# Optimization experiments

Hardware: AMD Instinct MI355X
Metric: run time of the kernel (lower is better)

## Reference

```python
import jax, jax.numpy as jnp
import numpy as np

INPUT_DIM, HIDDEN, EVENT_DIM = 64, 256, 32
B, T = 128, 1024


def setup_inputs() -> dict:
    key = jax.random.key(0)
    ks = jax.random.split(key, 20)
    s = 0.02
    return {
        "x": jax.random.normal(ks[0], (B, T, INPUT_DIM), jnp.float32),
        "events": jax.random.normal(ks[1], (B, T, EVENT_DIM), jnp.float32),
        "time_distances": jax.random.uniform(ks[2], (B, T), jnp.float32),
        # input projection
        "W_proj": s * jax.random.normal(ks[3], (INPUT_DIM, HIDDEN), jnp.float32),
        "b_proj": jnp.zeros((HIDDEN,), jnp.float32),
        # custom LSTM cell (input = projected_x of size HIDDEN)
        "W_ih": s * jax.random.normal(ks[4], (HIDDEN, 4 * HIDDEN), jnp.float32),
        "W_hh": s * jax.random.normal(ks[5], (HIDDEN, 4 * HIDDEN), jnp.float32),
        "b_lstm": jnp.zeros((4 * HIDDEN,), jnp.float32),
        # market-state gate from raw x
        "W_mk": s * jax.random.normal(ks[6], (INPUT_DIM, HIDDEN), jnp.float32),
        "b_mk": jnp.zeros((HIDDEN,), jnp.float32),
        # event processor
        "W_e": s * jax.random.normal(ks[7], (EVENT_DIM, HIDDEN), jnp.float32),
        "b_e": jnp.zeros((HIDDEN,), jnp.float32),
        "W_hg": s * jax.random.normal(ks[8], (HIDDEN, HIDDEN), jnp.float32),
        "b_hg": jnp.zeros((HIDDEN,), jnp.float32),
        "decay": jnp.asarray(0.5, jnp.float32),
        # predictor MLP (dropout is eval-mode identity)
        "W_p1": s * jax.random.normal(ks[9], (HIDDEN, HIDDEN // 2), jnp.float32),
        "b_p1": jnp.zeros((HIDDEN // 2,), jnp.float32),
        "W_p2": s * jax.random.normal(ks[10], (HIDDEN // 2, 1), jnp.float32),
        "b_p2": jnp.zeros((1,), jnp.float32),
    }


def _tmdo(x):
    # temporal first difference and Laplacian (second difference), zero-padded to [B,T,D]
    d1 = jnp.concatenate([jnp.zeros_like(x[:, :1]), x[:, 1:] - x[:, :-1]], axis=1)
    lap = jnp.concatenate(
        [jnp.zeros_like(x[:, :1]),
         x[:, 2:] - 2.0 * x[:, 1:-1] + x[:, :-2],
         jnp.zeros_like(x[:, :1])], axis=1)
    return d1, lap


def reference(x, events, time_distances, W_proj, b_proj, W_ih, W_hh, b_lstm,
              W_mk, b_mk, W_e, b_e, W_hg, b_hg, decay, W_p1, b_p1, W_p2, b_p2):
    bsz, seq_len, _ = x.shape
    H = W_proj.shape[1]
    tmdo_features, lap_features = _tmdo(x)

    h0 = jnp.zeros((bsz, H), x.dtype)
    c0 = jnp.zeros((bsz, H), x.dtype)

    def step(carry, inp):
        h, c = carry
        xt, et, dt = inp  # [B,D_in], [B,E], [B]
        px = xt @ W_proj + b_proj                                  # input_proj
        # event processor: embedded event * hidden gate * time decay
        e = jnp.tanh(et @ W_e + b_e)
        gate = jax.nn.sigmoid(h @ W_hg + b_hg)
        impact = e * gate * jnp.exp(-jax.nn.softplus(decay) * dt[:, None])
        # custom LSTM cell with market gate from raw x and event injection
        gates = px @ W_ih + h @ W_hh + b_lstm
        i_g, f_g, g_g, o_g = jnp.split(gates, 4, axis=-1)
        mk = jax.nn.sigmoid(xt @ W_mk + b_mk)
        c_new = jax.nn.sigmoid(f_g) * c + jax.nn.sigmoid(i_g) * jnp.tanh(g_g) \
                + mk * jnp.tanh(impact)
        h_new = jax.nn.sigmoid(o_g) * jnp.tanh(c_new)
        # predictor (exact GELU like torch nn.GELU; dropout = identity in eval)
        pred = jax.nn.gelu(h_new @ W_p1 + b_p1, approximate=False) @ W_p2 + b_p2
        return (h_new, c_new), (pred, h_new)

    xs = (jnp.swapaxes(x, 0, 1), jnp.swapaxes(events, 0, 1),
          jnp.swapaxes(time_distances, 0, 1))
    _, (preds, feats) = jax.lax.scan(step, (h0, c0), xs)
    predictions = jnp.swapaxes(preds, 0, 1)  # [B,T,1]
    features = jnp.swapaxes(feats, 0, 1)     # [B,T,H]
    return predictions, features, tmdo_features
```

## Files before the change

kernel.cpp:

```cpp
#include <hip/hip_runtime.h>
#include <hip/hip_bf16.h>
#include <hip/hip_fp16.h>
#include <math.h>

#define BB 128
#define TT 1024
#define DIN 64
#define HH 256
#define EE 32
#define BT (BB * TT)

typedef unsigned int uint;
typedef unsigned char uchar;
typedef _Float16 half2v __attribute__((ext_vector_type(2)));

__device__ __forceinline__ int dot4(uint a, uint b, int c) {
  return __builtin_amdgcn_sdot4((int)a, (int)b, c, false);
}
__device__ __forceinline__ uint pkh(float a, float b) {
  return __builtin_bit_cast(uint, __builtin_amdgcn_cvt_pkrtz(a, b));
}
__device__ __forceinline__ half2v uph(uint u) { return __builtin_bit_cast(half2v, u); }
__device__ __forceinline__ float fdot2u(uint a, uint b, float c) {
  return __builtin_amdgcn_fdot2(uph(a), uph(b), c, false);
}
#define IDPP(v, c) __builtin_amdgcn_mov_dpp((v), (c), 0xF, 0xF, true)
#define FDPP(v, c) __int_as_float(__builtin_amdgcn_mov_dpp(__float_as_int(v), (c), 0xF, 0xF, true))
__device__ __forceinline__ int qsum(int v) {
  v += IDPP(v, 0xB1);
  v += IDPP(v, 0x4E);
  return v;
}
__device__ __forceinline__ float rcp_f(float x) { return __builtin_amdgcn_rcpf(x); }
__device__ __forceinline__ float sigm(float x) { return rcp_f(1.0f + __expf(-x)); }
__device__ __forceinline__ float tanh_f(float x) {
  return 1.0f - 2.0f * rcp_f(__expf(2.0f * x) + 1.0f);
}

__global__ void fold_f32(const float* __restrict__ Wproj, const float* __restrict__ Wih,
                         float* __restrict__ Wfold) {
  int idx = blockIdx.x * blockDim.x + threadIdx.x;
  if (idx >= 64 * 1024) return;
  int d = idx >> 10, n = idx & 1023;
  float a = 0.f;
  for (int k = 0; k < 256; ++k) a += Wproj[d * 256 + k] * Wih[k * 1024 + n];
  Wfold[d * 1024 + n] = a;
}

__global__ void bfold_kernel(const float* __restrict__ bproj, const float* __restrict__ Wih,
                             const float* __restrict__ blstm, float* __restrict__ bfold) {
  int n = blockIdx.x * blockDim.x + threadIdx.x;
  if (n >= 1024) return;
  float a = blstm[n];
  for (int k = 0; k < 256; ++k) a += bproj[k] * Wih[k * 1024 + n];
  bfold[n] = a;
}

__global__ __launch_bounds__(1024) void quant_all(
    const float* __restrict__ Whh, const float* __restrict__ Whg,
    const float* __restrict__ Wfold, const float* __restrict__ Wmk,
    const float* __restrict__ We,
    uint* __restrict__ WhV, uint* __restrict__ WhL,
    uint* __restrict__ XQ, uint* __restrict__ EQ,
    float* __restrict__ scales) {
  const int bid = blockIdx.x, tid = threadIdx.x;
  const float* src;
  int nelem;
  switch (bid) {
    case 0: src = Whh;   nelem = 262144; break;
    case 1: src = Whg;   nelem = 65536;  break;
    case 2: src = Wfold; nelem = 65536;  break;
    case 3: src = Wmk;   nelem = 16384;  break;
    default: src = We;   nelem = 8192;   break;
  }
  float m = 0.f;
  for (int i = tid; i < nelem; i += 1024) m = fmaxf(m, fabsf(src[i]));
#pragma unroll
  for (int d = 1; d < 64; d <<= 1) m = fmaxf(m, __shfl_xor(m, d));
  __shared__ float wm[16];
  if ((tid & 63) == 0) wm[tid >> 6] = m;
  __syncthreads();
  float mg = wm[0];
#pragma unroll
  for (int i = 1; i < 16; ++i) mg = fmaxf(mg, wm[i]);
  mg = fmaxf(mg, 1e-8f);
  if (tid == 0) scales[bid] = mg * (1.0f / 127.0f);
  const float inv = 127.0f / mg;

  if (bid == 0) {
    for (int i = tid; i < 65536; i += 1024) {
      int C = i >> 4, r = i & 15;
      int c = C >> 2, q = C & 3, mI = r >> 2, mm = r & 3;
      int k4 = q * 16 + mI * 4 + mm;
      uint d = 0;
#pragma unroll
      for (int bb = 0; bb < 4; ++bb) {
        int qv = __float2int_rn(Whh[(4 * k4 + bb) * 1024 + c] * inv);
        qv = max(-127, min(127, qv));
        d |= ((uint)(qv & 0xff)) << (8 * bb);
      }
      WhV[i] = d;
    }
  } else if (bid == 1) {
    for (int i = tid; i < 16384; i += 1024) {
      int mm = i & 3, rest = i >> 2;
      int mI = rest >> 10, jq = rest & 1023;
      int j = jq >> 2, qq = jq & 3;
      int k4 = qq * 16 + mI * 4 + mm;
      uint d = 0;
#pragma unroll
      for (int bb = 0; bb < 4; ++bb) {
        int qv = __float2int_rn(Whg[(4 * k4 + bb) * 256 + j] * inv);
        qv = max(-127, min(127, qv));
        d |= ((uint)(qv & 0xff)) << (8 * bb);
      }
      WhL[i] = d;
    }
  } else if (bid == 2) {
    for (int i = tid; i < 16384; i += 1024) {
      int c = i >> 4, k4 = i & 15;
      uint d = 0;
#pragma unroll
      for (int bb = 0; bb < 4; ++bb) {
        int qv = __float2int_rn(Wfold[(4 * k4 + bb) * 1024 + c] * inv);
        qv = max(-127, min(127, qv));
        d |= ((uint)(qv & 0xff)) << (8 * bb);
      }
      XQ[i] = d;
    }
  } else if (bid == 3) {
    for (int i = tid; i < 4096; i += 1024) {
      int j = i >> 4, k4 = i & 15;
      uint d = 0;
#pragma unroll
      for (int bb = 0; bb < 4; ++bb) {
        int qv = __float2int_rn(Wmk[(4 * k4 + bb) * 256 + j] * inv);
        qv = max(-127, min(127, qv));
        d |= ((uint)(qv & 0xff)) << (8 * bb);
      }
      XQ[16384 + i] = d;
    }
  } else {
    for (int i = tid; i < 2048; i += 1024) {
      int c = i >> 3, k4 = i & 7;
      uint d = 0;
#pragma unroll
      for (int bb = 0; bb < 4; ++bb) {
        int qv = __float2int_rn(We[(4 * k4 + bb) * 256 + c] * inv);
        qv = max(-127, min(127, qv));
        d |= ((uint)(qv & 0xff)) << (8 * bb);
      }
      EQ[i] = d;
    }
  }
}

__global__ void pack_wp1h(const float* __restrict__ Wp1, uint* __restrict__ WQ) {
  int idx = blockIdx.x * blockDim.x + threadIdx.x;
  if (idx >= 16384) return;
  int j = idx >> 7, kp = idx & 127;
  WQ[idx] = pkh(Wp1[(2 * kp) * 128 + j], Wp1[(2 * kp + 1) * 128 + j]);
}

__global__ __launch_bounds__(256) void prep_inputs(
    const float* __restrict__ x, const float* __restrict__ ev, const float* __restrict__ td,
    const float* __restrict__ decay, uint* __restrict__ xq, uint* __restrict__ eq,
    float4* __restrict__ scl) {
  int wid = threadIdx.x >> 6, lane = threadIdx.x & 63;
  int bt = blockIdx.x * 4 + wid;
  if (bt >= BT) return;
  float xv = x[(size_t)bt * DIN + lane];
  float evv = (lane < EE) ? ev[(size_t)bt * EE + lane] : 0.0f;
  float ax = fabsf(xv), ae = fabsf(evv);
#pragma unroll
  for (int m = 1; m < 64; m <<= 1) {
    ax = fmaxf(ax, __shfl_xor(ax, m));
    ae = fmaxf(ae, __shfl_xor(ae, m));
  }
  float mgx = fmaxf(ax, 1e-8f), mge = fmaxf(ae, 1e-8f);
  int qx = __float2int_rn(xv * (127.0f / mgx));
  qx = max(-127, min(127, qx));
  int qe = __float2int_rn(evv * (127.0f / mge));
  qe = max(-127, min(127, qe));
  uint dx = 0, de = 0;
#pragma unroll
  for (int b = 0; b < 4; ++b) dx |= ((uint)(__shfl(qx, lane * 4 + b) & 0xff)) << (8 * b);
#pragma unroll
  for (int b = 0; b < 4; ++b) de |= ((uint)(__shfl(qe, lane * 4 + b) & 0xff)) << (8 * b);
  if (lane < 16) xq[(size_t)bt * 16 + lane] = dx;
  if (lane < 8) eq[(size_t)bt * 8 + lane] = de;
  if (lane == 0) {
    float sp = log1pf(__expf(decay[0]));
    scl[bt] = make_float4(mgx * (1.0f / 127.0f), mge * (1.0f / 127.0f),
                          __expf(-sp * td[bt]), 0.0f);
  }
}

__global__ void d1_kernel(const float* __restrict__ x, float* __restrict__ out2) {
  int idx = blockIdx.x * blockDim.x + threadIdx.x;
  const int per_t = DIN / 4;
  if (idx >= BB * TT * per_t) return;
  int t = (idx / per_t) % TT;
  float4 cur = reinterpret_cast<const float4*>(x)[idx];
  float4 res;
  if (t == 0) {
    res = make_float4(0.f, 0.f, 0.f, 0.f);
  } else {
    float4 prv = reinterpret_cast<const float4*>(x)[idx - per_t];
    res = make_float4(cur.x - prv.x, cur.y - prv.y, cur.z - prv.z, cur.w - prv.w);
  }
  reinterpret_cast<float4*>(out2)[idx] = res;
}

__global__ __launch_bounds__(1024) void pre_kernel(
    int t0, int lsteps,
    const uint* __restrict__ XQ, const uint* __restrict__ EQ,
    const float* __restrict__ scales, const float* __restrict__ bfold,
    const float* __restrict__ bmk, const float* __restrict__ be,
    const uint* __restrict__ xq, const uint* __restrict__ eqp,
    const float4* __restrict__ scl, uint4* __restrict__ pre) {
  const int tid = threadIdx.x;
  const int jj = tid >> 2, g = tid & 3;
  uint wx[16];
#pragma unroll
  for (int k = 0; k < 16; ++k) wx[k] = XQ[(g * 256 + jj) * 16 + k];
  uint wm[4];
#pragma unroll
  for (int k = 0; k < 4; ++k) wm[k] = XQ[16384 + jj * 16 + g * 4 + k];
  const uint we0 = EQ[jj * 8 + g * 2], we1 = EQ[jj * 8 + g * 2 + 1];
  const float sXF = scales[2], sMK = scales[3], sE = scales[4];
  const float bf = bfold[g * 256 + jj];
  const float bmkv = bmk[jj], bev = be[jj];
  const int steps = 1 << lsteps;

  for (int it = 0; it < 64; ++it) {
    const int idx = blockIdx.x * 64 + it;
    const int b = idx >> lsteps, tl = idx & (steps - 1);
    const int bt = b * TT + t0 + tl;
    const uint4* x4 = (const uint4*)(xq + (size_t)bt * 16);
    const uint4 X0 = x4[0], X1 = x4[1], X2 = x4[2], X3 = x4[3];
    const uint4 Xg = x4[g];
    const uint2 E0 = ((const uint2*)(eqp + (size_t)bt * 8))[g];
    const float4 sv = scl[bt];

    int ag = 0;
    ag = dot4(wx[0], X0.x, ag);  ag = dot4(wx[1], X0.y, ag);
    ag = dot4(wx[2], X0.z, ag);  ag = dot4(wx[3], X0.w, ag);
    ag = dot4(wx[4], X1.x, ag);  ag = dot4(wx[5], X1.y, ag);
    ag = dot4(wx[6], X1.z, ag);  ag = dot4(wx[7], X1.w, ag);
    ag = dot4(wx[8], X2.x, ag);  ag = dot4(wx[9], X2.y, ag);
    ag = dot4(wx[10], X2.z, ag); ag = dot4(wx[11], X2.w, ag);
    ag = dot4(wx[12], X3.x, ag); ag = dot4(wx[13], X3.y, ag);
    ag = dot4(wx[14], X3.z, ag); ag = dot4(wx[15], X3.w, ag);

    int am = 0;
    am = dot4(wm[0], Xg.x, am); am = dot4(wm[1], Xg.y, am);
    am = dot4(wm[2], Xg.z, am); am = dot4(wm[3], Xg.w, am);
    int ae = dot4(we0, E0.x, 0);
    ae = dot4(we1, E0.y, ae);
    am = qsum(am);
    ae = qsum(ae);

    const float p = (float)ag * (sXF * sv.x) + bf;
    const float p1 = FDPP(p, 0x55);
    const float p2 = FDPP(p, 0xAA);
    const float p3 = FDPP(p, 0xFF);
    if (g == 0) {
      const float mkS = sigm((float)am * (sMK * sv.x) + bmkv);
      const float ge = (float)ae * (sE * sv.y) + bev;
      const float EF = tanh_f(ge) * sv.z;
      uint4 o;
      o.x = pkh(p, p1);
      o.y = pkh(p2, p3);
      o.z = __float_as_uint(mkS);
      o.w = __float_as_uint(EF);
      pre[(size_t)idx * 256 + jj] = o;
    }
  }
}

__attribute__((amdgpu_waves_per_eu(4, 4)))
__global__ __launch_bounds__(1024) void scan3(
    int t0, int steps,
    const uint* __restrict__ WhV, const uint* __restrict__ WhLg,
    const float* __restrict__ scales, const float* __restrict__ bhg,
    const uint4* __restrict__ pre, uchar* __restrict__ hB, float* __restrict__ cB,
    float* __restrict__ feat) {
  __shared__ __align__(16) uint WL[16384];
  __shared__ __align__(16) uint hqW[128];
  const int tid = threadIdx.x, b = blockIdx.x;
  const int j = tid >> 2, q = tid & 3;

  for (int i = tid; i < 4096; i += 1024) ((uint4*)WL)[i] = ((const uint4*)WhLg)[i];

  uint4 wh[4][4];
  const uint4* wv = (const uint4*)WhV;
#pragma unroll
  for (int g = 0; g < 4; ++g)
#pragma unroll
    for (int m = 0; m < 4; ++m) wh[g][m] = wv[(g * 1024 + tid) * 4 + m];

  float c;
  if (t0 == 0) {
    c = 0.0f;
    if (tid < 64) hqW[tid] = 0u;
  } else {
    c = cB[b * 256 + j];
    if (tid < 64) hqW[tid] = ((const uint*)hB)[b * 64 + tid];
  }
  const float kHH = scales[0] * (1.0f / 127.0f);
  const float kHG = scales[1] * (1.0f / 127.0f);
  const float bhgv = bhg[j];
  const uint4* prep = pre + (size_t)b * steps * 256;
  float* fout = feat + ((size_t)b * TT + t0) * HH;
  const uint4* WL4 = (const uint4*)WL;
  int buf = 0;
  __syncthreads();

  uint4 P = prep[j];
  for (int t = 0; t < steps; ++t) {
    uint4 Pn = P;
    if (t + 1 < steps) Pn = prep[(size_t)(t + 1) * 256 + j];

    int a0 = 0, a1 = 0, a2 = 0, a3 = 0, a4 = 0;
    const uint4* hp = (const uint4*)((const uchar*)hqW + buf * 256 + q * 64);
#pragma unroll
    for (int m = 0; m < 4; ++m) {
      const uint4 hv = hp[m];
      const uint4 wg = WL4[m * 1024 + tid];
      a0 = dot4(wh[0][m].x, hv.x, a0); a0 = dot4(wh[0][m].y, hv.y, a0);
      a0 = dot4(wh[0][m].z, hv.z, a0); a0 = dot4(wh[0][m].w, hv.w, a0);
      a1 = dot4(wh[1][m].x, hv.x, a1); a1 = dot4(wh[1][m].y, hv.y, a1);
      a1 = dot4(wh[1][m].z, hv.z, a1); a1 = dot4(wh[1][m].w, hv.w, a1);
      a2 = dot4(wh[2][m].x, hv.x, a2); a2 = dot4(wh[2][m].y, hv.y, a2);
      a2 = dot4(wh[2][m].z, hv.z, a2); a2 = dot4(wh[2][m].w, hv.w, a2);
      a3 = dot4(wh[3][m].x, hv.x, a3); a3 = dot4(wh[3][m].y, hv.y, a3);
      a3 = dot4(wh[3][m].z, hv.z, a3); a3 = dot4(wh[3][m].w, hv.w, a3);
      a4 = dot4(wg.x, hv.x, a4);       a4 = dot4(wg.y, hv.y, a4);
      a4 = dot4(wg.z, hv.z, a4);       a4 = dot4(wg.w, hv.w, a4);
    }
    a0 = qsum(a0); a1 = qsum(a1); a2 = qsum(a2); a3 = qsum(a3); a4 = qsum(a4);

    const half2v pif = uph(P.x), pgo = uph(P.y);
    const float p0 = (float)a0 * kHH + (float)pif.x;
    const float p1 = (float)a1 * kHH + (float)pif.y;
    const float p2 = (float)a2 * kHH + (float)pgo.x;
    const float p3 = (float)a3 * kHH + (float)pgo.y;
    const float p4 = (float)a4 * kHG + bhgv;
    const float mkS = __uint_as_float(P.z);
    const float EF = __uint_as_float(P.w);

    const float impact = EF * sigm(p4);
    c = sigm(p1) * c + sigm(p0) * tanh_f(p2) + mkS * tanh_f(impact);
    const float hn = sigm(p3) * tanh_f(c);

    if (q == 0) {
      fout[(size_t)t * HH + j] = hn;
      int qi = __float2int_rn(hn * 127.0f);
      ((uchar*)hqW)[(buf ^ 1) * 256 + j] = (uchar)(qi & 0xff);
    }
    __syncthreads();
    buf ^= 1;
    P = Pn;
  }
  if (q == 0) cB[b * 256 + j] = c;
  if (tid < 64) ((uint*)hB)[b * 64 + tid] = hqW[buf * 64 + tid];
}

__global__ __launch_bounds__(256) void pred3(
    const float* __restrict__ feat, const uint* __restrict__ WQh,
    const float* __restrict__ bp1, const float* __restrict__ Wp2,
    const float* __restrict__ bp2, float* __restrict__ out0) {
  __shared__ uint WL[16384];
  __shared__ uint hT[128 * 132];
  __shared__ float psum[4][128];

  const int tid = threadIdx.x, w = tid >> 6, l = tid & 63;
  const int rbase = blockIdx.x * 128;

  for (int i = tid; i < 16384; i += 256) WL[i] = WQh[i];
  for (int i = tid; i < 16384; i += 256) {
    int row = i >> 7, kp = i & 127;
    const float2 hv = ((const float2*)feat)[(size_t)(rbase + row) * 128 + kp];
    hT[row * 132 + kp] = pkh(hv.x, hv.y);
  }
  __syncthreads();

  float ma[32], mb[32];
#pragma unroll
  for (int jj = 0; jj < 32; ++jj) {
    const float bv = bp1[w * 32 + jj];
    ma[jj] = bv;
    mb[jj] = bv;
  }
  const uint* ha = &hT[l * 132];
  const uint* hb = &hT[(l + 64) * 132];
  const uint* wbase = &WL[(w * 32) * 128];
  for (int kp4 = 0; kp4 < 32; ++kp4) {
    const uint4 a4 = *(const uint4*)&ha[kp4 * 4];
    const uint4 b4 = *(const uint4*)&hb[kp4 * 4];
#pragma unroll
    for (int jj = 0; jj < 32; ++jj) {
      const uint4 w4 = *(const uint4*)&wbase[jj * 128 + kp4 * 4];
      ma[jj] = fdot2u(w4.x, a4.x, ma[jj]);
      ma[jj] = fdot2u(w4.y, a4.y, ma[jj]);
      ma[jj] = fdot2u(w4.z, a4.z, ma[jj]);
      ma[jj] = fdot2u(w4.w, a4.w, ma[jj]);
      mb[jj] = fdot2u(w4.x, b4.x, mb[jj]);
      mb[jj] = fdot2u(w4.y, b4.y, mb[jj]);
      mb[jj] = fdot2u(w4.z, b4.z, mb[jj]);
      mb[jj] = fdot2u(w4.w, b4.w, mb[jj]);
    }
  }
  float accA = 0.f, accB = 0.f;
#pragma unroll
  for (int jj = 0; jj < 32; ++jj) {
    const float w2v = Wp2[w * 32 + jj];
    accA += 0.5f * ma[jj] * (1.0f + erff(ma[jj] * 0.70710678118f)) * w2v;
    accB += 0.5f * mb[jj] * (1.0f + erff(mb[jj] * 0.70710678118f)) * w2v;
  }
  psum[w][l] = accA;
  psum[w][64 + l] = accB;
  __syncthreads();
  if (tid < 128)
    out0[rbase + tid] =
        psum[0][tid] + psum[1][tid] + psum[2][tid] + psum[3][tid] + bp2[0];
}

extern "C" void kernel_launch(void* const* d_in, const int* in_sizes, int n_in,
                              void* d_out, int out_size, void* d_ws, size_t ws_size,
                              hipStream_t stream) {
  const float* x = (const float*)d_in[0];
  const float* ev = (const float*)d_in[1];
  const float* td = (const float*)d_in[2];
  const float* Wproj = (const float*)d_in[3];
  const float* bproj = (const float*)d_in[4];
  const float* Wih = (const float*)d_in[5];
  const float* Whh = (const float*)d_in[6];
  const float* blstm = (const float*)d_in[7];
  const float* Wmk = (const float*)d_in[8];
  const float* bmk = (const float*)d_in[9];
  const float* We = (const float*)d_in[10];
  const float* be = (const float*)d_in[11];
  const float* Whg = (const float*)d_in[12];
  const float* bhg = (const float*)d_in[13];
  const float* decay = (const float*)d_in[14];
  const float* Wp1 = (const float*)d_in[15];
  const float* bp1 = (const float*)d_in[16];
  const float* Wp2 = (const float*)d_in[17];
  const float* bp2 = (const float*)d_in[18];

  float* out0 = (float*)d_out;
  float* out1 = out0 + (size_t)BT;
  float* out2 = out1 + (size_t)BT * HH;

  char* w = (char*)d_ws;
  float* Wfold_f = (float*)w; w += (size_t)65536 * 4;
  uint* WhV = (uint*)w; w += (size_t)65536 * 4;
  uint* WhL = (uint*)w; w += (size_t)16384 * 4;
  uint* XQ = (uint*)w; w += (size_t)20480 * 4;
  uint* EQ = (uint*)w; w += (size_t)2048 * 4;
  uint* WQh = (uint*)w; w += (size_t)16384 * 4;
  float* scales = (float*)w; w += 16 * 4;
  float* bfold = (float*)w; w += 1024 * 4;
  uchar* hB = (uchar*)w; w += (size_t)BB * 256;
  float* cB = (float*)w; w += (size_t)BB * 256 * 4;
  uint* xq = (uint*)w; w += (size_t)BT * 16 * 4;
  uint* eq = (uint*)w; w += (size_t)BT * 8 * 4;
  float4* scl = (float4*)w; w += (size_t)BT * 16;
  uint4* pre = (uint4*)w;

  size_t used = (size_t)(w - (char*)d_ws);
  size_t avail = (ws_size > used + 4096) ? (ws_size - used - 4096) : 0;
  int steps = TT, lsteps = 10;
  while (steps > 4 && (size_t)BB * (size_t)steps * 256 * 16 > avail) {
    steps >>= 1;
    lsteps--;
  }

  hipLaunchKernelGGL(fold_f32, dim3(256), dim3(256), 0, stream, Wproj, Wih, Wfold_f);
  hipLaunchKernelGGL(bfold_kernel, dim3(4), dim3(256), 0, stream, bproj, Wih, blstm, bfold);
  hipLaunchKernelGGL(quant_all, dim3(5), dim3(1024), 0, stream,
                     Whh, Whg, Wfold_f, Wmk, We, WhV, WhL, XQ, EQ, scales);
  hipLaunchKernelGGL(pack_wp1h, dim3(64), dim3(256), 0, stream, Wp1, WQh);
  hipLaunchKernelGGL(prep_inputs, dim3(BT / 4), dim3(256), 0, stream,
                     x, ev, td, decay, xq, eq, scl);
  hipLaunchKernelGGL(d1_kernel, dim3(8192), dim3(256), 0, stream, x, out2);

  for (int t0 = 0; t0 < TT; t0 += steps) {
    hipLaunchKernelGGL(pre_kernel, dim3(2 * steps), dim3(1024), 0, stream,
                       t0, lsteps, XQ, EQ, scales, bfold, bmk, be, xq, eq, scl, pre);
    hipLaunchKernelGGL(scan3, dim3(BB), dim3(1024), 0, stream,
                       t0, steps, WhV, WhL, scales, bhg, pre, hB, cB, out1);
  }

  hipLaunchKernelGGL(pred3, dim3(BT / 128), dim3(256), 0, stream,
                     out1, WQh, bp1, Wp2, bp2, out0);
}
```

Measured before the change: 2.109 ms.

## Keep hidden-gate weights in registers and split input projection by K-quarter

```diff
diff --git a/kernel.cpp b/kernel.cpp
--- a/kernel.cpp
+++ b/kernel.cpp
@@ -25,7 +25,6 @@
   return __builtin_amdgcn_fdot2(uph(a), uph(b), c, false);
 }
 #define IDPP(v, c) __builtin_amdgcn_mov_dpp((v), (c), 0xF, 0xF, true)
-#define FDPP(v, c) __int_as_float(__builtin_amdgcn_mov_dpp(__float_as_int(v), (c), 0xF, 0xF, true))
 __device__ __forceinline__ int qsum(int v) {
   v += IDPP(v, 0xB1);
   v += IDPP(v, 0x4E);
@@ -60,8 +59,7 @@
     const float* __restrict__ Whh, const float* __restrict__ Whg,
     const float* __restrict__ Wfold, const float* __restrict__ Wmk,
     const float* __restrict__ We,
-    uint* __restrict__ WhV, uint* __restrict__ WhL,
-    uint* __restrict__ XQ, uint* __restrict__ EQ,
+    uint* __restrict__ WhQ, uint* __restrict__ XQ, uint* __restrict__ EQ,
     float* __restrict__ scales) {
   const int bid = blockIdx.x, tid = threadIdx.x;
   const float* src;
@@ -99,14 +97,13 @@
         qv = max(-127, min(127, qv));
         d |= ((uint)(qv & 0xff)) << (8 * bb);
       }
-      WhV[i] = d;
+      WhQ[i] = d;
     }
   } else if (bid == 1) {
     for (int i = tid; i < 16384; i += 1024) {
-      int mm = i & 3, rest = i >> 2;
-      int mI = rest >> 10, jq = rest & 1023;
-      int j = jq >> 2, qq = jq & 3;
-      int k4 = qq * 16 + mI * 4 + mm;
+      int j = i >> 6, rr = i & 63;
+      int q = rr >> 4, mI = (rr >> 2) & 3, mm = rr & 3;
+      int k4 = q * 16 + mI * 4 + mm;
       uint d = 0;
 #pragma unroll
       for (int bb = 0; bb < 4; ++bb) {
@@ -114,7 +111,7 @@
         qv = max(-127, min(127, qv));
         d |= ((uint)(qv & 0xff)) << (8 * bb);
       }
-      WhL[i] = d;
+      WhQ[65536 + i] = d;
     }
   } else if (bid == 2) {
     for (int i = tid; i < 16384; i += 1024) {
@@ -212,7 +209,7 @@
   reinterpret_cast<float4*>(out2)[idx] = res;
 }
 
-__global__ __launch_bounds__(1024) void pre_kernel(
+__global__ __launch_bounds__(1024) void pre2(
     int t0, int lsteps,
     const uint* __restrict__ XQ, const uint* __restrict__ EQ,
     const float* __restrict__ scales, const float* __restrict__ bfold,
@@ -220,85 +217,81 @@
     const uint* __restrict__ xq, const uint* __restrict__ eqp,
     const float4* __restrict__ scl, uint4* __restrict__ pre) {
   const int tid = threadIdx.x;
-  const int jj = tid >> 2, g = tid & 3;
-  uint wx[16];
-#pragma unroll
-  for (int k = 0; k < 16; ++k) wx[k] = XQ[(g * 256 + jj) * 16 + k];
-  uint wm[4];
-#pragma unroll
-  for (int k = 0; k < 4; ++k) wm[k] = XQ[16384 + jj * 16 + g * 4 + k];
-  const uint we0 = EQ[jj * 8 + g * 2], we1 = EQ[jj * 8 + g * 2 + 1];
+  const int j = tid >> 2, q = tid & 3;
+
+  uint4 wx[4];
+#pragma unroll
+  for (int g = 0; g < 4; ++g)
+    wx[g] = *(const uint4*)(XQ + (g * 256 + j) * 16 + q * 4);
+  const uint4 wmv = *(const uint4*)(XQ + 16384 + j * 16 + q * 4);
+  const uint2 wev = *(const uint2*)(EQ + j * 8 + q * 2);
+  float bf[4];
+#pragma unroll
+  for (int g = 0; g < 4; ++g) bf[g] = bfold[g * 256 + j];
+  const float bmkv = bmk[j], bev = be[j];
   const float sXF = scales[2], sMK = scales[3], sE = scales[4];
-  const float bf = bfold[g * 256 + jj];
-  const float bmkv = bmk[jj], bev = be[jj];
   const int steps = 1 << lsteps;
 
   for (int it = 0; it < 64; ++it) {
     const int idx = blockIdx.x * 64 + it;
     const int b = idx >> lsteps, tl = idx & (steps - 1);
     const int bt = b * TT + t0 + tl;
-    const uint4* x4 = (const uint4*)(xq + (size_t)bt * 16);
-    const uint4 X0 = x4[0], X1 = x4[1], X2 = x4[2], X3 = x4[3];
-    const uint4 Xg = x4[g];
-    const uint2 E0 = ((const uint2*)(eqp + (size_t)bt * 8))[g];
+    const uint4 X = *(const uint4*)(xq + (size_t)bt * 16 + q * 4);
+    const uint2 E = *(const uint2*)(eqp + (size_t)bt * 8 + q * 2);
     const float4 sv = scl[bt];
 
-    int ag = 0;
-    ag = dot4(wx[0], X0.x, ag);  ag = dot4(wx[1], X0.y, ag);
-    ag = dot4(wx[2], X0.z, ag);  ag = dot4(wx[3], X0.w, ag);
-    ag = dot4(wx[4], X1.x, ag);  ag = dot4(wx[5], X1.y, ag);
-    ag = dot4(wx[6], X1.z, ag);  ag = dot4(wx[7], X1.w, ag);
-    ag = dot4(wx[8], X2.x, ag);  ag = dot4(wx[9], X2.y, ag);
-    ag = dot4(wx[10], X2.z, ag); ag = dot4(wx[11], X2.w, ag);
-    ag = dot4(wx[12], X3.x, ag); ag = dot4(wx[13], X3.y, ag);
-    ag = dot4(wx[14], X3.z, ag); ag = dot4(wx[15], X3.w, ag);
-
-    int am = 0;
-    am = dot4(wm[0], Xg.x, am); am = dot4(wm[1], Xg.y, am);
-    am = dot4(wm[2], Xg.z, am); am = dot4(wm[3], Xg.w, am);
-    int ae = dot4(we0, E0.x, 0);
-    ae = dot4(we1, E0.y, ae);
-    am = qsum(am);
-    ae = qsum(ae);
-
-    const float p = (float)ag * (sXF * sv.x) + bf;
-    const float p1 = FDPP(p, 0x55);
-    const float p2 = FDPP(p, 0xAA);
-    const float p3 = FDPP(p, 0xFF);
-    if (g == 0) {
+    int a0 = 0, a1 = 0, a2 = 0, a3 = 0, am = 0, ae = 0;
+    a0 = dot4(wx[0].x, X.x, a0); a0 = dot4(wx[0].y, X.y, a0);
+    a0 = dot4(wx[0].z, X.z, a0); a0 = dot4(wx[0].w, X.w, a0);
+    a1 = dot4(wx[1].x, X.x, a1); a1 = dot4(wx[1].y, X.y, a1);
+    a1 = dot4(wx[1].z, X.z, a1); a1 = dot4(wx[1].w, X.w, a1);
+    a2 = dot4(wx[2].x, X.x, a2); a2 = dot4(wx[2].y, X.y, a2);
+    a2 = dot4(wx[2].z, X.z, a2); a2 = dot4(wx[2].w, X.w, a2);
+    a3 = dot4(wx[3].x, X.x, a3); a3 = dot4(wx[3].y, X.y, a3);
+    a3 = dot4(wx[3].z, X.z, a3); a3 = dot4(wx[3].w, X.w, a3);
+    am = dot4(wmv.x, X.x, am);   am = dot4(wmv.y, X.y, am);
+    am = dot4(wmv.z, X.z, am);   am = dot4(wmv.w, X.w, am);
+    ae = dot4(wev.x, E.x, ae);   ae = dot4(wev.y, E.y, ae);
+
+    a0 = qsum(a0); a1 = qsum(a1); a2 = qsum(a2);
+    a3 = qsum(a3); am = qsum(am); ae = qsum(ae);
+
+    if (q == 0) {
+      const float fx = sXF * sv.x;
+      const float p0 = (float)a0 * fx + bf[0];
+      const float p1 = (float)a1 * fx + bf[1];
+      const float p2 = (float)a2 * fx + bf[2];
+      const float p3 = (float)a3 * fx + bf[3];
       const float mkS = sigm((float)am * (sMK * sv.x) + bmkv);
-      const float ge = (float)ae * (sE * sv.y) + bev;
-      const float EF = tanh_f(ge) * sv.z;
+      const float EF = tanh_f((float)ae * (sE * sv.y) + bev) * sv.z;
       uint4 o;
-      o.x = pkh(p, p1);
+      o.x = pkh(p0, p1);
       o.y = pkh(p2, p3);
       o.z = __float_as_uint(mkS);
       o.w = __float_as_uint(EF);
-      pre[(size_t)idx * 256 + jj] = o;
-    }
-  }
-}
-
-__attribute__((amdgpu_waves_per_eu(4, 4)))
+      pre[(size_t)idx * 256 + j] = o;
+    }
+  }
+}
+
 __global__ __launch_bounds__(1024) void scan3(
-    int t0, int steps,
-    const uint* __restrict__ WhV, const uint* __restrict__ WhLg,
+    int t0, int steps, const uint* __restrict__ WhQ,
     const float* __restrict__ scales, const float* __restrict__ bhg,
     const uint4* __restrict__ pre, uchar* __restrict__ hB, float* __restrict__ cB,
     float* __restrict__ feat) {
-  __shared__ __align__(16) uint WL[16384];
   __shared__ __align__(16) uint hqW[128];
   const int tid = threadIdx.x, b = blockIdx.x;
   const int j = tid >> 2, q = tid & 3;
 
-  for (int i = tid; i < 4096; i += 1024) ((uint4*)WL)[i] = ((const uint4*)WhLg)[i];
-
+  const uint4* wv = (const uint4*)WhQ;
   uint4 wh[4][4];
-  const uint4* wv = (const uint4*)WhV;
 #pragma unroll
   for (int g = 0; g < 4; ++g)
 #pragma unroll
-    for (int m = 0; m < 4; ++m) wh[g][m] = wv[(g * 1024 + tid) * 4 + m];
+    for (int m = 0; m < 4; ++m) wh[g][m] = wv[((g * 256 + j) * 4 + q) * 4 + m];
+  uint4 wg[4];
+#pragma unroll
+  for (int m = 0; m < 4; ++m) wg[m] = wv[((1024 + j) * 4 + q) * 4 + m];
 
   float c;
   if (t0 == 0) {
@@ -313,7 +306,6 @@
   const float bhgv = bhg[j];
   const uint4* prep = pre + (size_t)b * steps * 256;
   float* fout = feat + ((size_t)b * TT + t0) * HH;
-  const uint4* WL4 = (const uint4*)WL;
   int buf = 0;
   __syncthreads();
 
@@ -327,7 +319,6 @@
 #pragma unroll
     for (int m = 0; m < 4; ++m) {
       const uint4 hv = hp[m];
-      const uint4 wg = WL4[m * 1024 + tid];
       a0 = dot4(wh[0][m].x, hv.x, a0); a0 = dot4(wh[0][m].y, hv.y, a0);
       a0 = dot4(wh[0][m].z, hv.z, a0); a0 = dot4(wh[0][m].w, hv.w, a0);
       a1 = dot4(wh[1][m].x, hv.x, a1); a1 = dot4(wh[1][m].y, hv.y, a1);
@@ -336,8 +327,8 @@
       a2 = dot4(wh[2][m].z, hv.z, a2); a2 = dot4(wh[2][m].w, hv.w, a2);
       a3 = dot4(wh[3][m].x, hv.x, a3); a3 = dot4(wh[3][m].y, hv.y, a3);
       a3 = dot4(wh[3][m].z, hv.z, a3); a3 = dot4(wh[3][m].w, hv.w, a3);
-      a4 = dot4(wg.x, hv.x, a4);       a4 = dot4(wg.y, hv.y, a4);
-      a4 = dot4(wg.z, hv.z, a4);       a4 = dot4(wg.w, hv.w, a4);
+      a4 = dot4(wg[m].x, hv.x, a4);    a4 = dot4(wg[m].y, hv.y, a4);
+      a4 = dot4(wg[m].z, hv.z, a4);    a4 = dot4(wg[m].w, hv.w, a4);
     }
     a0 = qsum(a0); a1 = qsum(a1); a2 = qsum(a2); a3 = qsum(a3); a4 = qsum(a4);
 
@@ -456,8 +447,7 @@
 
   char* w = (char*)d_ws;
   float* Wfold_f = (float*)w; w += (size_t)65536 * 4;
-  uint* WhV = (uint*)w; w += (size_t)65536 * 4;
-  uint* WhL = (uint*)w; w += (size_t)16384 * 4;
+  uint* WhQ = (uint*)w; w += (size_t)81920 * 4;
   uint* XQ = (uint*)w; w += (size_t)20480 * 4;
   uint* EQ = (uint*)w; w += (size_t)2048 * 4;
   uint* WQh = (uint*)w; w += (size_t)16384 * 4;
@@ -481,17 +471,17 @@
   hipLaunchKernelGGL(fold_f32, dim3(256), dim3(256), 0, stream, Wproj, Wih, Wfold_f);
   hipLaunchKernelGGL(bfold_kernel, dim3(4), dim3(256), 0, stream, bproj, Wih, blstm, bfold);
   hipLaunchKernelGGL(quant_all, dim3(5), dim3(1024), 0, stream,
-                     Whh, Whg, Wfold_f, Wmk, We, WhV, WhL, XQ, EQ, scales);
+                     Whh, Whg, Wfold_f, Wmk, We, WhQ, XQ, EQ, scales);
   hipLaunchKernelGGL(pack_wp1h, dim3(64), dim3(256), 0, stream, Wp1, WQh);
   hipLaunchKernelGGL(prep_inputs, dim3(BT / 4), dim3(256), 0, stream,
                      x, ev, td, decay, xq, eq, scl);
   hipLaunchKernelGGL(d1_kernel, dim3(8192), dim3(256), 0, stream, x, out2);
 
   for (int t0 = 0; t0 < TT; t0 += steps) {
-    hipLaunchKernelGGL(pre_kernel, dim3(2 * steps), dim3(1024), 0, stream,
+    hipLaunchKernelGGL(pre2, dim3(2 * steps), dim3(1024), 0, stream,
                        t0, lsteps, XQ, EQ, scales, bfold, bmk, be, xq, eq, scl, pre);
     hipLaunchKernelGGL(scan3, dim3(BB), dim3(1024), 0, stream,
-                       t0, steps, WhV, WhL, scales, bhg, pre, hB, cB, out1);
+                       t0, steps, WhQ, scales, bhg, pre, hB, cB, out1);
   }
 
   hipLaunchKernelGGL(pred3, dim3(BT / 128), dim3(256), 0, stream,
```

Measured after the change: 2.114 ms. No clear change (+0.3%).
